# Kernel tuning notes

Measured on AMD Instinct MI355X. Metric: run time of the kernel, lower is better.

The kernel has to match this reference:

```python
import jax, jax.numpy as jnp
import numpy as np

SEQ_LEN, BATCH, INPUT_SIZE, HIDDEN = 2048, 64, 256, 512


def setup_inputs() -> dict:
    key = jax.random.key(0)
    ks = jax.random.split(key, 6)
    s_i = 1.0 / np.sqrt(HIDDEN)
    return {
        "x": jax.random.normal(ks[0], (SEQ_LEN, BATCH, INPUT_SIZE), dtype=jnp.float32),
        "keep_mask": jax.random.randint(ks[1], (HIDDEN,), 0, 2, dtype=jnp.int32),
        # PyTorch nn.LSTM params, gate order (i, f, g, o) stacked on dim 0
        "W_ih": jax.random.uniform(ks[2], (4 * HIDDEN, INPUT_SIZE), jnp.float32, -s_i, s_i),
        "W_hh": jax.random.uniform(ks[3], (4 * HIDDEN, HIDDEN), jnp.float32, -s_i, s_i),
        "b_ih": jax.random.uniform(ks[4], (4 * HIDDEN,), jnp.float32, -s_i, s_i),
        "b_hh": jax.random.uniform(ks[5], (4 * HIDDEN,), jnp.float32, -s_i, s_i),
    }


def _masked_lstm(x, keep_mask, W_ih, W_hh, b_ih, b_hh):
    H = W_hh.shape[1]
    keep = keep_mask.astype(bool)  # [H]; h channels where keep==False are zeroed each step
    # precompute input contribution for all timesteps: [T, B, 4H]
    x_gates = jnp.einsum("tbi,gi->tbg", x, W_ih) + b_ih + b_hh

    def step(carry, xg_t):
        h, c = carry  # [B, H] each
        gates = xg_t + h @ W_hh.T  # [B, 4H]
        i, f, g, o = jnp.split(gates, 4, axis=-1)
        c = jax.nn.sigmoid(f) * c + jax.nn.sigmoid(i) * jnp.tanh(g)
        h = jax.nn.sigmoid(o) * jnp.tanh(c)
        h = jnp.where(keep, h, 0.0)  # mask applied to h BEFORE it feeds next step
        return (h, c), h

    B = x.shape[1]
    h0 = jnp.zeros((B, H), x.dtype)
    c0 = jnp.zeros((B, H), x.dtype)
    (h_t, c_t), output = jax.lax.scan(step, (h0, c0), x_gates)
    return output, h_t, c_t


def reference(x, keep_mask, W_ih, W_hh, b_ih, b_hh):
    output, h_t, c_t = _masked_lstm(x, keep_mask, W_ih, W_hh, b_ih, b_hh)
    # match torch module: (output [T,B,H], (h_n [1,B,H], c_n [1,B,H]))
    return output, (h_t[None], c_t[None])
```

## Files before the change

kernel.cpp:

```cpp
#include <hip/hip_runtime.h>

#define T_STEPS 2048
#define NBATCH  64
#define ISZ     256
#define HID     512
#define BH      (NBATCH*HID)

typedef __attribute__((ext_vector_type(8))) __bf16 bf16x8;
typedef __attribute__((ext_vector_type(4))) float  f32x4;
typedef __attribute__((ext_vector_type(4))) unsigned int u32x4;

#define MFMA __builtin_amdgcn_mfma_f32_16x16x32_bf16

__device__ __forceinline__ float sigm(float v){ return 1.0f/(1.0f+expf(-v)); }

__device__ __forceinline__ unsigned int pack2(__bf16 a, __bf16 b){
    return (unsigned int)__builtin_bit_cast(unsigned short,a)
         | ((unsigned int)__builtin_bit_cast(unsigned short,b)<<16);
}

__global__ void __launch_bounds__(256,1)
lstm_persist(const float* __restrict__ x, const int* __restrict__ keep,
             const float* __restrict__ Wih, const float* __restrict__ Whh,
             const float* __restrict__ bih, const float* __restrict__ bhh,
             float* __restrict__ outp, unsigned int* __restrict__ wsbuf)
{
    __shared__ float G[4][8][32];
    __shared__ float C[8][32];
    __shared__ __align__(16) char XB[2][8][1024];
    __shared__ __align__(16) char HXs[8][1024];

    const int tid=threadIdx.x, wv=tid>>6, lane=tid&63, bid=blockIdx.x;
    const int g=bid&7, w=bid>>3, ch0=w*32, bbase=g*8;
    const int n=lane&15, lg=lane>>4, nr=(n<8)?n:7;

    unsigned int* tags = wsbuf;
    unsigned int* ex32 = wsbuf + 2048;

    bf16x8 whh0[2][16], whh1[2][16], wih0[2][8], wih1[2][8];
    float biasv[2];
#pragma unroll
    for (int nt=0; nt<2; ++nt){
        const int row = wv*HID + ch0 + nt*16 + n;
        const float* wr = Whh + (size_t)row*HID + lg*8;
#pragma unroll
        for (int kt=0; kt<16; ++kt){
            const float* p = wr + kt*32;
            bf16x8 b0,b1;
#pragma unroll
            for(int e=0;e<8;++e){
                float f=p[e]; __bf16 hh=(__bf16)f;
                b0[e]=hh; b1[e]=(__bf16)(f-(float)hh);
            }
            whh0[nt][kt]=b0; whh1[nt][kt]=b1;
        }
        const float* wr2 = Wih + (size_t)row*ISZ + lg*8;
#pragma unroll
        for (int kt=0; kt<8; ++kt){
            const float* p = wr2 + kt*32;
            bf16x8 b0,b1;
#pragma unroll
            for(int e=0;e<8;++e){
                float f=p[e]; __bf16 hh=(__bf16)f;
                b0[e]=hh; b1[e]=(__bf16)(f-(float)hh);
            }
            wih0[nt][kt]=b0; wih1[nt][kt]=b1;
        }
        biasv[nt] = bih[row] + bhh[row];
    }

    const int erow = tid>>5, ech = tid&31;
    const int kp = keep[ch0 + ech];
    C[erow][ech] = 0.0f;

    const int c64 = tid&63, row0 = tid>>6, row1 = row0+4;

    {
        const char* s0 = (const char*)x + ((size_t)(bbase+row0)*ISZ)*4 + (size_t)c64*16;
        const char* s1 = (const char*)x + ((size_t)(bbase+row1)*ISZ)*4 + (size_t)c64*16;
        u32x4 q0 = *(const u32x4*)s0, q1 = *(const u32x4*)s1;
        *(u32x4*)&XB[0][row0][(c64^row0)*16] = q0;
        *(u32x4*)&XB[0][row1][(c64^row1)*16] = q1;
    }
    __syncthreads();

    unsigned int* mytag = tags + (size_t)(g*16+w)*16;
    unsigned int* gtags = tags + (size_t)g*16*16;

    for (int t=0; t<T_STEPS; ++t){
        const bool hasx = (t+1<T_STEPS);
        u32x4 xq0, xq1;
        if (hasx){
            const char* s0 = (const char*)x + (((size_t)(t+1)*NBATCH + bbase+row0)*ISZ)*4 + (size_t)c64*16;
            const char* s1 = (const char*)x + (((size_t)(t+1)*NBATCH + bbase+row1)*ISZ)*4 + (size_t)c64*16;
            xq0 = *(const u32x4*)s0;
            xq1 = *(const u32x4*)s1;
        }

        f32x4 a0v[2] = {{biasv[0],biasv[0],biasv[0],biasv[0]},
                        {biasv[1],biasv[1],biasv[1],biasv[1]}};
        f32x4 a1v[2] = {{0,0,0,0},{0,0,0,0}};
#pragma unroll
        for (int kt2=0; kt2<8; ++kt2){
            f32x4 xa = *(const f32x4*)&XB[t&1][nr][(((kt2*8)+lg*2+0)^nr)*16];
            f32x4 xb = *(const f32x4*)&XB[t&1][nr][(((kt2*8)+lg*2+1)^nr)*16];
            bf16x8 a0,a1;
#pragma unroll
            for(int e=0;e<4;++e){
                float f=xa[e]; __bf16 hh=(__bf16)f;
                a0[e]=hh; a1[e]=(__bf16)(f-(float)hh);
                f=xb[e]; hh=(__bf16)f;
                a0[e+4]=hh; a1[e+4]=(__bf16)(f-(float)hh);
            }
            a0v[0]=MFMA(a0,wih0[0][kt2],a0v[0],0,0,0);
            a0v[1]=MFMA(a0,wih0[1][kt2],a0v[1],0,0,0);
            a1v[0]=MFMA(a0,wih1[0][kt2],a1v[0],0,0,0);
            a1v[1]=MFMA(a0,wih1[1][kt2],a1v[1],0,0,0);
            a1v[0]=MFMA(a1,wih0[0][kt2],a1v[0],0,0,0);
            a1v[1]=MFMA(a1,wih0[1][kt2],a1v[1],0,0,0);
        }

        if (t>0){
            const unsigned int need=(unsigned int)t;
            while(1){
                unsigned int v=need;
                if (lane<16)
                    v=__hip_atomic_load(gtags+lane*16,__ATOMIC_RELAXED,__HIP_MEMORY_SCOPE_AGENT);
                if (__all(v>=need)) break;
                __builtin_amdgcn_s_sleep(1);
                asm volatile("" ::: "memory");
            }
            asm volatile("" ::: "memory");
        }

        u32x4 hq0, hq1;
        if (t>0){
            const unsigned long long* e64 =
                (const unsigned long long*)(ex32 + (size_t)(g*2 + ((t-1)&1))*2048);
            unsigned long long a = __hip_atomic_load(e64 + tid*2,        __ATOMIC_RELAXED, __HIP_MEMORY_SCOPE_AGENT);
            unsigned long long b = __hip_atomic_load(e64 + tid*2+1,      __ATOMIC_RELAXED, __HIP_MEMORY_SCOPE_AGENT);
            unsigned long long c = __hip_atomic_load(e64 + (tid+256)*2,  __ATOMIC_RELAXED, __HIP_MEMORY_SCOPE_AGENT);
            unsigned long long d = __hip_atomic_load(e64 + (tid+256)*2+1,__ATOMIC_RELAXED, __HIP_MEMORY_SCOPE_AGENT);
            hq0[0]=(unsigned int)a; hq0[1]=(unsigned int)(a>>32); hq0[2]=(unsigned int)b; hq0[3]=(unsigned int)(b>>32);
            hq1[0]=(unsigned int)c; hq1[1]=(unsigned int)(c>>32); hq1[2]=(unsigned int)d; hq1[3]=(unsigned int)(d>>32);
        }
        asm volatile("s_waitcnt vmcnt(0)" ::: "memory");
        __builtin_amdgcn_sched_barrier(0);
        if (t>0){
            *(u32x4*)&HXs[row0][(c64^row0)*16] = hq0;
            *(u32x4*)&HXs[row1][(c64^row1)*16] = hq1;
        }
        if (hasx){
            *(u32x4*)&XB[(t+1)&1][row0][(c64^row0)*16] = xq0;
            *(u32x4*)&XB[(t+1)&1][row1][(c64^row1)*16] = xq1;
        }
        __syncthreads();

        if (t>0){
#pragma unroll
            for (int kt=0;kt<16;++kt){
                bf16x8 h0 = *(const bf16x8*)&HXs[nr][(((kt*4)+lg)^nr)*16];
                a0v[0]=MFMA(h0,whh0[0][kt],a0v[0],0,0,0);
                a0v[1]=MFMA(h0,whh0[1][kt],a0v[1],0,0,0);
                a1v[0]=MFMA(h0,whh1[0][kt],a1v[0],0,0,0);
                a1v[1]=MFMA(h0,whh1[1][kt],a1v[1],0,0,0);
            }
        }

        if (lane<32){
#pragma unroll
            for (int nt=0; nt<2; ++nt){
                f32x4 acc = a0v[nt]+a1v[nt];
#pragma unroll
                for(int r=0;r<4;++r) G[wv][lg*4+r][nt*16+n]=acc[r];
            }
        }
        __syncthreads();

        float gi=G[0][erow][ech], gf=G[1][erow][ech], gg=G[2][erow][ech], go=G[3][erow][ech];
        float cc = sigm(gf)*C[erow][ech] + sigm(gi)*tanhf(gg);
        C[erow][ech]=cc;
        float hh = sigm(go)*tanhf(cc); if(!kp) hh=0.0f;

        float hnb = __shfl_xor(hh, 1);
        if (!(tid&1)){
            unsigned int pk = pack2((__bf16)hh, (__bf16)hnb);
            unsigned int* ea = ex32 + (size_t)(g*2+(t&1))*2048 + erow*256 + ((ch0+ech)>>1);
            __hip_atomic_store(ea, pk, __ATOMIC_RELAXED, __HIP_MEMORY_SCOPE_AGENT);
        }
        asm volatile("s_waitcnt vmcnt(0)" ::: "memory");
        __syncthreads();

        if (tid==0)
            __hip_atomic_store(mytag,(unsigned int)(t+1),__ATOMIC_RELAXED,__HIP_MEMORY_SCOPE_AGENT);

        outp[(size_t)t*BH + (size_t)(bbase+erow)*HID + ch0+ech] = hh;
        if (t==T_STEPS-1){
            outp[(size_t)T_STEPS*BH + (size_t)(bbase+erow)*HID + ch0+ech]      = hh;
            outp[(size_t)T_STEPS*BH + BH + (size_t)(bbase+erow)*HID + ch0+ech] = cc;
        }
    }
}

__global__ void lstm_init_tags(unsigned int* tags)
{
    int i = blockIdx.x*256 + threadIdx.x;
    if (i < 128*16)
        __hip_atomic_store(tags+i, 0u, __ATOMIC_RELAXED, __HIP_MEMORY_SCOPE_AGENT);
}

extern "C" void kernel_launch(void* const* d_in, const int* in_sizes, int n_in,
                              void* d_out, int out_size, void* d_ws, size_t ws_size,
                              hipStream_t stream)
{
    const void *px = nullptr, *pk = nullptr, *pwi = nullptr, *pwh = nullptr,
               *pb0 = nullptr, *pb1 = nullptr;
    for (int i = 0; i < n_in; ++i) {
        const long s = (long)in_sizes[i];
        if      (s == (long)T_STEPS * NBATCH * ISZ) px  = d_in[i];
        else if (s == HID)                          pk  = d_in[i];
        else if (s == 4L * HID * ISZ)               pwi = d_in[i];
        else if (s == 4L * HID * HID)               pwh = d_in[i];
        else if (s == 4L * HID) { if (!pb0) pb0 = d_in[i]; else pb1 = d_in[i]; }
    }
    if (!px || !pk || !pwi || !pwh || !pb0 || !pb1) {
        px = d_in[0]; pk = d_in[1]; pwi = d_in[2]; pwh = d_in[3]; pb0 = d_in[4]; pb1 = d_in[5];
    }

    lstm_init_tags<<<dim3(8), dim3(256), 0, stream>>>((unsigned int*)d_ws);
    lstm_persist<<<dim3(128), dim3(256), 0, stream>>>(
        (const float*)px, (const int*)pk, (const float*)pwi, (const float*)pwh,
        (const float*)pb0, (const float*)pb1, (float*)d_out, (unsigned int*)d_ws);
}
```

Measured before the change: 7.164 ms.

## Stamp exchanged hidden-state words with step counter, dropping separate tag flags

```diff
diff --git a/kernel.cpp b/kernel.cpp
--- a/kernel.cpp
+++ b/kernel.cpp
@@ -23,7 +23,7 @@
 lstm_persist(const float* __restrict__ x, const int* __restrict__ keep,
              const float* __restrict__ Wih, const float* __restrict__ Whh,
              const float* __restrict__ bih, const float* __restrict__ bhh,
-             float* __restrict__ outp, unsigned int* __restrict__ wsbuf)
+             float* __restrict__ outp, unsigned long long* __restrict__ exch)
 {
     __shared__ float G[4][8][32];
     __shared__ float C[8][32];
@@ -34,8 +34,6 @@
     const int g=bid&7, w=bid>>3, ch0=w*32, bbase=g*8;
     const int n=lane&15, lg=lane>>4, nr=(n<8)?n:7;
 
-    unsigned int* tags = wsbuf;
-    unsigned int* ex32 = wsbuf + 2048;
 
     bf16x8 whh0[2][16], whh1[2][16], wih0[2][8], wih1[2][8];
     float biasv[2];
@@ -83,9 +81,6 @@
         *(u32x4*)&XB[0][row1][(c64^row1)*16] = q1;
     }
     __syncthreads();
-
-    unsigned int* mytag = tags + (size_t)(g*16+w)*16;
-    unsigned int* gtags = tags + (size_t)g*16*16;
 
     for (int t=0; t<T_STEPS; ++t){
         const bool hasx = (t+1<T_STEPS);
@@ -120,32 +115,32 @@
             a1v[1]=MFMA(a1,wih0[1][kt2],a1v[1],0,0,0);
         }
 
-        if (t>0){
-            const unsigned int need=(unsigned int)t;
-            while(1){
-                unsigned int v=need;
-                if (lane<16)
-                    v=__hip_atomic_load(gtags+lane*16,__ATOMIC_RELAXED,__HIP_MEMORY_SCOPE_AGENT);
-                if (__all(v>=need)) break;
-                __builtin_amdgcn_s_sleep(1);
-                asm volatile("" ::: "memory");
-            }
-            asm volatile("" ::: "memory");
-        }
-
         u32x4 hq0, hq1;
         if (t>0){
-            const unsigned long long* e64 =
-                (const unsigned long long*)(ex32 + (size_t)(g*2 + ((t-1)&1))*2048);
-            unsigned long long a = __hip_atomic_load(e64 + tid*2,        __ATOMIC_RELAXED, __HIP_MEMORY_SCOPE_AGENT);
-            unsigned long long b = __hip_atomic_load(e64 + tid*2+1,      __ATOMIC_RELAXED, __HIP_MEMORY_SCOPE_AGENT);
-            unsigned long long c = __hip_atomic_load(e64 + (tid+256)*2,  __ATOMIC_RELAXED, __HIP_MEMORY_SCOPE_AGENT);
-            unsigned long long d = __hip_atomic_load(e64 + (tid+256)*2+1,__ATOMIC_RELAXED, __HIP_MEMORY_SCOPE_AGENT);
-            hq0[0]=(unsigned int)a; hq0[1]=(unsigned int)(a>>32); hq0[2]=(unsigned int)b; hq0[3]=(unsigned int)(b>>32);
-            hq1[0]=(unsigned int)c; hq1[1]=(unsigned int)(c>>32); hq1[2]=(unsigned int)d; hq1[3]=(unsigned int)(d>>32);
-        }
-        asm volatile("s_waitcnt vmcnt(0)" ::: "memory");
-        __builtin_amdgcn_sched_barrier(0);
+            const unsigned int need = (unsigned int)t;
+            const unsigned long long* e64 = exch + (size_t)(g*2 + ((t-1)&1))*2048;
+            unsigned long long q[8];
+            while(1){
+#pragma unroll
+                for (int j=0;j<4;++j)
+                    q[j]   = __hip_atomic_load(e64 + (size_t)tid*4 + j,
+                                               __ATOMIC_RELAXED, __HIP_MEMORY_SCOPE_AGENT);
+#pragma unroll
+                for (int j=0;j<4;++j)
+                    q[4+j] = __hip_atomic_load(e64 + (size_t)(tid+256)*4 + j,
+                                               __ATOMIC_RELAXED, __HIP_MEMORY_SCOPE_AGENT);
+                bool ok = true;
+#pragma unroll
+                for (int j=0;j<8;++j) ok &= ((unsigned int)(q[j]>>32) == need);
+                if (ok) break;
+                __builtin_amdgcn_s_sleep(1);
+            }
+            hq0[0]=(unsigned int)q[0]; hq0[1]=(unsigned int)q[1];
+            hq0[2]=(unsigned int)q[2]; hq0[3]=(unsigned int)q[3];
+            hq1[0]=(unsigned int)q[4]; hq1[1]=(unsigned int)q[5];
+            hq1[2]=(unsigned int)q[6]; hq1[3]=(unsigned int)q[7];
+        }
+
         if (t>0){
             *(u32x4*)&HXs[row0][(c64^row0)*16] = hq0;
             *(u32x4*)&HXs[row1][(c64^row1)*16] = hq1;
@@ -184,15 +179,11 @@
 
         float hnb = __shfl_xor(hh, 1);
         if (!(tid&1)){
-            unsigned int pk = pack2((__bf16)hh, (__bf16)hnb);
-            unsigned int* ea = ex32 + (size_t)(g*2+(t&1))*2048 + erow*256 + ((ch0+ech)>>1);
-            __hip_atomic_store(ea, pk, __ATOMIC_RELAXED, __HIP_MEMORY_SCOPE_AGENT);
-        }
-        asm volatile("s_waitcnt vmcnt(0)" ::: "memory");
-        __syncthreads();
-
-        if (tid==0)
-            __hip_atomic_store(mytag,(unsigned int)(t+1),__ATOMIC_RELAXED,__HIP_MEMORY_SCOPE_AGENT);
+            unsigned long long val = ((unsigned long long)(unsigned int)(t+1) << 32)
+                                   | (unsigned long long)pack2((__bf16)hh, (__bf16)hnb);
+            __hip_atomic_store(exch + (size_t)(g*2+(t&1))*2048 + erow*256 + ((ch0+ech)>>1),
+                               val, __ATOMIC_RELAXED, __HIP_MEMORY_SCOPE_AGENT);
+        }
 
         outp[(size_t)t*BH + (size_t)(bbase+erow)*HID + ch0+ech] = hh;
         if (t==T_STEPS-1){
@@ -200,13 +191,6 @@
             outp[(size_t)T_STEPS*BH + BH + (size_t)(bbase+erow)*HID + ch0+ech] = cc;
         }
     }
-}
-
-__global__ void lstm_init_tags(unsigned int* tags)
-{
-    int i = blockIdx.x*256 + threadIdx.x;
-    if (i < 128*16)
-        __hip_atomic_store(tags+i, 0u, __ATOMIC_RELAXED, __HIP_MEMORY_SCOPE_AGENT);
 }
 
 extern "C" void kernel_launch(void* const* d_in, const int* in_sizes, int n_in,
@@ -227,8 +211,8 @@
         px = d_in[0]; pk = d_in[1]; pwi = d_in[2]; pwh = d_in[3]; pb0 = d_in[4]; pb1 = d_in[5];
     }
 
-    lstm_init_tags<<<dim3(8), dim3(256), 0, stream>>>((unsigned int*)d_ws);
     lstm_persist<<<dim3(128), dim3(256), 0, stream>>>(
         (const float*)px, (const int*)pk, (const float*)pwi, (const float*)pwh,
-        (const float*)pb0, (const float*)pb1, (float*)d_out, (unsigned int*)d_ws);
+        (const float*)pb0, (const float*)pb1, (float*)d_out,
+        (unsigned long long*)d_ws);
 }
```

Measured after the change: 6.689 ms, median of 2. 6.6% less time.
